# Kernel optimization log

Measured on AMD Instinct MI355X. Metric: run time of the kernel, lower is better.

Reference implementation:

```python
import jax, jax.numpy as jnp
import numpy as np

N = 100_000          # nodes
E = 1_600_000        # edges (avg degree 16)
F_RAW = 124          # float feature columns (after id column removed)
ID_DIM = 4
NF = F_RAW + ID_DIM  # encoder input features = 128
EMB = 64             # embedding_size, heads=1
L = 4                # num_layers
VOCAB = 2048         # id embedding table size
GAT_SLOPE = 0.2      # GATv2 attention leaky slope (PyG default)
ACT_SLOPE = 0.01     # nn.LeakyReLU default
EPS = 1e-5           # GraphNorm eps


def setup_inputs() -> dict:
    key = jax.random.key(0)
    ks = jax.random.split(key, 12)
    x_feat = jax.random.normal(ks[0], (N, F_RAW), jnp.float32)
    node_ids = jax.random.randint(ks[1], (N,), 0, VOCAB)
    edge_index = jax.random.randint(ks[2], (2, E), 0, N)
    emb_table = jax.random.normal(ks[3], (VOCAB, ID_DIM), jnp.float32) * 0.1
    w_in = jax.random.normal(ks[4], (NF, EMB), jnp.float32) / np.sqrt(NF)
    b_in = jnp.zeros((EMB,), jnp.float32)
    lin_w = jax.random.normal(ks[5], (L, EMB, EMB), jnp.float32) / np.sqrt(EMB)
    lin_b = jnp.zeros((L, EMB), jnp.float32)
    att = jax.random.normal(ks[6], (L, EMB), jnp.float32) / np.sqrt(EMB)
    conv_b = jnp.zeros((L, EMB), jnp.float32)
    gn_w = jnp.ones((L, EMB), jnp.float32)
    gn_b = jnp.zeros((L, EMB), jnp.float32)
    gn_ms = jnp.ones((L, EMB), jnp.float32)  # GraphNorm mean_scale
    return {"x_feat": x_feat, "node_ids": node_ids, "edge_index": edge_index,
            "emb_table": emb_table, "w_in": w_in, "b_in": b_in,
            "lin_w": lin_w, "lin_b": lin_b, "att": att, "conv_b": conv_b,
            "gn_w": gn_w, "gn_b": gn_b, "gn_ms": gn_ms}


def reference(x_feat, node_ids, edge_index, emb_table, w_in, b_in,
              lin_w, lin_b, att, conv_b, gn_w, gn_b, gn_ms):
    # id_encode: embedding lookup + concat with float features
    x = jnp.concatenate([x_feat, emb_table[node_ids]], axis=1)  # [N, 128]
    # encoder input projection (BatchNorm skipped: remove_random=True)
    x = jax.nn.leaky_relu(x @ w_in + b_in, ACT_SLOPE)           # [N, 64]
    n = x.shape[0]
    loops = jnp.arange(n)
    src = jnp.concatenate([edge_index[0], loops])               # add self loops
    dst = jnp.concatenate([edge_index[1], loops])
    h = None
    xs = []
    for l in range(L):
        # GATv2Conv, heads=1, share_weights=True (one shared linear)
        g = x @ lin_w[l] + lin_b[l]                             # [N, 64]
        e = jax.nn.leaky_relu(g[src] + g[dst], GAT_SLOPE) @ att[l]  # [E+N]
        # segment softmax over incoming edges per target node
        m = jax.ops.segment_max(e, dst, num_segments=n)
        ee = jnp.exp(e - m[dst])
        s = jax.ops.segment_sum(ee, dst, num_segments=n)
        alpha = ee / s[dst]                                     # [E+N]
        xs.append(alpha)
        x = jax.ops.segment_sum(alpha[:, None] * g[src], dst, num_segments=n) + conv_b[l]
        # GraphNorm (single graph: batch=None)
        mean = jnp.mean(x, axis=0)
        out = x - mean * gn_ms[l]
        var = jnp.mean(out * out, axis=0)
        x = out / jnp.sqrt(var + EPS) * gn_w[l] + gn_b[l]
        x = jax.nn.leaky_relu(x, ACT_SLOPE)
        # dropout p=0.3 is identity at inference
        h = x * 0.5 if h is None else h + x * 0.5
    return x, h, jnp.stack(xs, axis=0)  # ([N,64], [N,64], [L, E+N])
```

## Files before the change

kernel.cpp:

```cpp
#include <hip/hip_runtime.h>
#include <hip/hip_bf16.h>
#include <cstdint>

typedef __hip_bfloat16 bf16;
#define DEVI __device__ __forceinline__

DEVI float b2f(bf16 v){ return __bfloat162float(v); }
DEVI bf16 f2b(float v){ return __float2bfloat16(v); }
DEVI float lrelu(float x, float s){ return x > 0.f ? x : x * s; }

DEVI float ldf(const void* p, size_t i, int f){
  return f ? b2f(((const bf16*)p)[i]) : ((const float*)p)[i];
}
DEVI void stf(void* p, size_t i, int f, float v){
  if(f) ((bf16*)p)[i] = f2b(v); else ((float*)p)[i] = v;
}

DEVI float wave_sum(float v){
#pragma unroll
  for(int o = 32; o > 0; o >>= 1) v += __shfl_xor(v, o, 64);
  return v;
}
DEVI float qsum(float v){
  v += __shfl_xor(v, 1, 64);
  v += __shfl_xor(v, 2, 64);
  v += __shfl_xor(v, 4, 64);
  v += __shfl_xor(v, 8, 64);
  return v;
}

__global__ void k_detect(const uint32_t* __restrict__ xf, int* flag){
  const int lane = threadIdx.x & 63;
  float cnt = 0.f;
  for(int i = lane; i < 256; i += 64){
    uint32_t e = (xf[i] >> 7) & 0xFF;
    if(e >= 100 && e <= 140) cnt += 1.f;
  }
  cnt = wave_sum(cnt);
  if(lane == 0 && blockIdx.x == 0) *flag = (cnt > 180.f) ? 1 : 0;
}

__global__ __launch_bounds__(256) void k_encoder(
    const void* __restrict__ xf, const int* __restrict__ ids,
    const void* __restrict__ emb, const void* __restrict__ win,
    const void* __restrict__ bin, float* __restrict__ x,
    const int* __restrict__ flagp, int N)
{
  __shared__ float W[128*64];
  __shared__ float B[64];
  __shared__ float XR[4][128];
  const int t = threadIdx.x;
  const int f = *flagp;
  for(int i = t; i < 128*64; i += 256) W[i] = ldf(win, i, f);
  if(t < 64) B[t] = ldf(bin, t, f);
  __syncthreads();
  const int w = t >> 6, lane = t & 63;
  for(int base = blockIdx.x*4; base < N; base += gridDim.x*4){
    const int node = base + w;
    if(node < N){
      for(int k = lane; k < 128; k += 64){
        float v;
        if(k < 124) v = ldf(xf, (size_t)node*124 + k, f);
        else        v = ldf(emb, (size_t)ids[node]*4 + (k-124), f);
        XR[w][k] = v;
      }
      float acc = B[lane];
#pragma unroll 8
      for(int k = 0; k < 128; k++) acc = fmaf(XR[w][k], W[k*64+lane], acc);
      x[(size_t)node*64 + lane] = lrelu(acc, 0.01f);
    }
  }
}

__global__ __launch_bounds__(256) void k_linear(
    const float* __restrict__ x, const void* __restrict__ lw,
    const void* __restrict__ lb, float* __restrict__ g,
    const int* __restrict__ flagp, int layer, int N)
{
  __shared__ float W[64*64];
  __shared__ float B[64];
  __shared__ float XR[4][64];
  const int t = threadIdx.x;
  const int f = *flagp;
  const size_t wofs = (size_t)layer*64*64, bofs = (size_t)layer*64;
  for(int i = t; i < 64*64; i += 256) W[i] = ldf(lw, wofs + i, f);
  if(t < 64) B[t] = ldf(lb, bofs + t, f);
  __syncthreads();
  const int w = t >> 6, lane = t & 63;
  for(int base = blockIdx.x*4; base < N; base += gridDim.x*4){
    const int node = base + w;
    if(node < N){
      XR[w][lane] = x[(size_t)node*64 + lane];
      float acc = B[lane];
#pragma unroll 8
      for(int k = 0; k < 64; k++) acc = fmaf(XR[w][k], W[k*64+lane], acc);
      g[(size_t)node*64 + lane] = acc;
    }
  }
}

__global__ void k_deg_init(int* deg, int N){
  int i = blockIdx.x*blockDim.x + threadIdx.x;
  if(i < N) deg[i] = 1;
}
__global__ void k_deg_count(const int* __restrict__ dst, int* deg, int E){
  int j = blockIdx.x*blockDim.x + threadIdx.x;
  if(j < E) atomicAdd(&deg[dst[j]], 1);
}
__global__ __launch_bounds__(256) void k_scan_partial(const int* __restrict__ deg, int* partial, int N){
  __shared__ int red[256];
  const int c = blockIdx.x, base = c*1024, t = threadIdx.x;
  int s = 0;
  for(int i = t; i < 1024; i += 256){ int idx = base+i; s += (idx < N) ? deg[idx] : 0; }
  red[t] = s; __syncthreads();
  for(int o = 128; o > 0; o >>= 1){ if(t < o) red[t] += red[t+o]; __syncthreads(); }
  if(t == 0) partial[c] = red[0];
}
__global__ void k_scan_top(int* partial, int nchunks){
  if(threadIdx.x == 0 && blockIdx.x == 0){
    int run = 0;
    for(int i = 0; i < nchunks; i++){ int v = partial[i]; partial[i] = run; run += v; }
  }
}
__global__ __launch_bounds__(256) void k_scan_final(
    const int* __restrict__ deg, const int* __restrict__ partial,
    int* __restrict__ off, int* __restrict__ cur, int N)
{
  __shared__ int vals[1024];
  __shared__ int tsum[256];
  const int c = blockIdx.x, base = c*1024, t = threadIdx.x;
  for(int i = t; i < 1024; i += 256){ int idx = base+i; vals[i] = (idx < N) ? deg[idx] : 0; }
  __syncthreads();
  int a0 = vals[t*4], a1 = vals[t*4+1], a2 = vals[t*4+2], a3 = vals[t*4+3];
  int s = a0+a1+a2+a3;
  tsum[t] = s; __syncthreads();
  for(int o = 1; o < 256; o <<= 1){
    int v = (t >= o) ? tsum[t-o] : 0;
    __syncthreads();
    tsum[t] += v;
    __syncthreads();
  }
  int excl = tsum[t] - s + partial[c];
  int o0 = excl, o1 = o0+a0, o2 = o1+a1, o3 = o2+a2;
  int idx = base + t*4;
  if(idx   < N){ off[idx]   = o0; cur[idx]   = o0; }
  if(idx+1 < N){ off[idx+1] = o1; cur[idx+1] = o1; }
  if(idx+2 < N){ off[idx+2] = o2; cur[idx+2] = o2; }
  if(idx+3 < N){ off[idx+3] = o3; cur[idx+3] = o3; }
}
__global__ void k_scatter(const int* __restrict__ src, const int* __restrict__ dst,
                          int* cur, int* __restrict__ pos, int* __restrict__ csrc,
                          int E, int N){
  int j = blockIdx.x*blockDim.x + threadIdx.x;
  int T = E + N;
  if(j >= T) return;
  int s, d;
  if(j < E){ s = src[j]; d = dst[j]; } else { s = j - E; d = s; }
  int p = atomicAdd(&cur[d], 1);
  csrc[p] = s;
  pos[j]  = p;
}

__global__ __launch_bounds__(256) void k_gat(
    const float* __restrict__ g, const int* __restrict__ off,
    const int* __restrict__ deg, const int* __restrict__ csrc,
    const void* __restrict__ att, const void* __restrict__ convb,
    float* __restrict__ xout, float* __restrict__ acsr,
    float* __restrict__ stats, const int* __restrict__ flagp,
    int layer, int N)
{
  __shared__ float sv[4][64], sv2[4][64];
  const int t = threadIdx.x, w = t >> 6, lane = t & 63;
  const int q = lane >> 4, L = lane & 15;
  const int f = *flagp;
  const size_t pofs = (size_t)layer*64;
  const int node = blockIdx.x*4 + w;
  const bool act = node < N;
  const int nc = act ? node : (N-1);

  float4 attv, cbv;
  attv.x = ldf(att, pofs + 4*L+0, f); attv.y = ldf(att, pofs + 4*L+1, f);
  attv.z = ldf(att, pofs + 4*L+2, f); attv.w = ldf(att, pofs + 4*L+3, f);
  cbv.x = ldf(convb, pofs + 4*L+0, f); cbv.y = ldf(convb, pofs + 4*L+1, f);
  cbv.z = ldf(convb, pofs + 4*L+2, f); cbv.w = ldf(convb, pofs + 4*L+3, f);

  const float4 gd = *(const float4*)(g + (size_t)nc*64 + 4*L);
  const int o = off[nc];
  const int d = act ? deg[nc] : 0;
  const int sreg = csrc[o + (lane < d ? lane : 0)];

  float m = -1e30f, sp = 0.f, ereg = -1e30f;
  float4 acc = {0.f, 0.f, 0.f, 0.f};
  const int nit = (d + 3) >> 2;

  float4 gs;
  {
    const int s0 = __shfl(sreg, q, 64);
    gs = *(const float4*)(g + (size_t)s0*64 + 4*L);
  }
  for(int i = 0; i < nit; i++){
    float4 gnx = {0.f, 0.f, 0.f, 0.f};
    const int i1 = i + 1;
    const bool more = i1 < nit;
    if(more){
      int sn;
      if(i1 < 16) sn = __shfl(sreg, i1*4 + q, 64);
      else { const int j2 = i1*4 + q; sn = csrc[o + (j2 < d ? j2 : 0)]; }
      gnx = *(const float4*)(g + (size_t)sn*64 + 4*L);
    }
    const int j = i*4 + q;
    const bool have = j < d;
    float pe = lrelu(gs.x+gd.x, 0.2f)*attv.x + lrelu(gs.y+gd.y, 0.2f)*attv.y
             + lrelu(gs.z+gd.z, 0.2f)*attv.z + lrelu(gs.w+gd.w, 0.2f)*attv.w;
    float e = qsum(pe);
    if(!have) e = -1e30f;
    ereg = (L == i) ? e : ereg;
    const float mn = fmaxf(m, e);
    const float sc = __expf(m - mn);
    const float wt = __expf(e - mn);
    sp    = sp*sc    + wt;
    acc.x = acc.x*sc + wt*gs.x;
    acc.y = acc.y*sc + wt*gs.y;
    acc.z = acc.z*sc + wt*gs.z;
    acc.w = acc.w*sc + wt*gs.w;
    m = mn;
    if(more) gs = gnx;
  }
#pragma unroll
  for(int ofs = 16; ofs <= 32; ofs <<= 1){
    const float m2  = __shfl_xor(m,  ofs, 64);
    const float sp2 = __shfl_xor(sp, ofs, 64);
    float4 a2;
    a2.x = __shfl_xor(acc.x, ofs, 64); a2.y = __shfl_xor(acc.y, ofs, 64);
    a2.z = __shfl_xor(acc.z, ofs, 64); a2.w = __shfl_xor(acc.w, ofs, 64);
    const float mn = fmaxf(m, m2);
    const float sA = __expf(m - mn), sB = __expf(m2 - mn);
    sp    = sp*sA    + sp2*sB;
    acc.x = acc.x*sA + a2.x*sB;
    acc.y = acc.y*sA + a2.y*sB;
    acc.z = acc.z*sA + a2.z*sB;
    acc.w = acc.w*sA + a2.w*sB;
    m = mn;
  }
  const float inv = 1.f / sp;

  if(act){
    const int j = 4*L + q;
    if(j < d && j < 64)
      acsr[o + j] = __expf(ereg - m) * inv;
    for(int i = 16; i < nit; i++){
      const int j2 = i*4 + q;
      const bool have = j2 < d;
      const int s = csrc[o + (have ? j2 : 0)];
      const float4 gs2 = *(const float4*)(g + (size_t)s*64 + 4*L);
      float pe = lrelu(gs2.x+gd.x, 0.2f)*attv.x + lrelu(gs2.y+gd.y, 0.2f)*attv.y
               + lrelu(gs2.z+gd.z, 0.2f)*attv.z + lrelu(gs2.w+gd.w, 0.2f)*attv.w;
      float e = qsum(pe);
      if(have && L == 0)
        acsr[o + j2] = __expf(e - m) * inv;
    }
  }
  float4 v4 = {0.f, 0.f, 0.f, 0.f};
  if(act){
    v4.x = acc.x*inv + cbv.x; v4.y = acc.y*inv + cbv.y;
    v4.z = acc.z*inv + cbv.z; v4.w = acc.w*inv + cbv.w;
    if(q == 0) *(float4*)(xout + (size_t)node*64 + 4*L) = v4;
  }
  if(q == 0){
    sv [w][4*L+0] = v4.x;      sv [w][4*L+1] = v4.y;
    sv [w][4*L+2] = v4.z;      sv [w][4*L+3] = v4.w;
    sv2[w][4*L+0] = v4.x*v4.x; sv2[w][4*L+1] = v4.y*v4.y;
    sv2[w][4*L+2] = v4.z*v4.z; sv2[w][4*L+3] = v4.w*v4.w;
  }
  __syncthreads();
  if(w == 0){
    float a = sv[0][lane]+sv[1][lane]+sv[2][lane]+sv[3][lane];
    float b = sv2[0][lane]+sv2[1][lane]+sv2[2][lane]+sv2[3][lane];
    const int bank = (blockIdx.x & 7) * 128;
    atomicAdd(&stats[bank + lane],      a);
    atomicAdd(&stats[bank + 64 + lane], b);
  }
}

__global__ __launch_bounds__(256) void k_alpha_out(
    const float* __restrict__ acsr, const int* __restrict__ pos,
    void* __restrict__ out, size_t alpha_base,
    const int* __restrict__ flagp, int T)
{
  const int f = *flagp;
  for(size_t j = (size_t)blockIdx.x*256 + threadIdx.x; j < (size_t)T;
      j += (size_t)gridDim.x*256){
    stf(out, alpha_base + j, f, acsr[pos[j]]);
  }
}

__global__ void k_zero_stats(float* stats){ stats[threadIdx.x] = 0.f; }

__global__ __launch_bounds__(256) void k_gn_apply(
    float* __restrict__ x, const float* __restrict__ stats,
    const void* __restrict__ gw, const void* __restrict__ gb,
    const void* __restrict__ gms, void* __restrict__ out,
    size_t x_base, size_t h_base, const int* __restrict__ flagp,
    int N, int layer, float invN)
{
  const int f = *flagp;
  const int lane = threadIdx.x & 63;
  const size_t pofs = (size_t)layer*64;
  float s1 = 0.f, s2 = 0.f;
#pragma unroll
  for(int c = 0; c < 8; c++){
    s1 += stats[c*128 + lane];
    s2 += stats[c*128 + 64 + lane];
  }
  const float mean = s1 * invN;
  const float ex2  = s2 * invN;
  const float c    = mean * ldf(gms, pofs + lane, f);
  const float var  = ex2 - 2.f*c*mean + c*c;
  const float a    = ldf(gw, pofs + lane, f) / sqrtf(var + 1e-5f);
  const float bb   = ldf(gb, pofs + lane, f);
  const size_t total = (size_t)N * 64;
  for(size_t idx = (size_t)blockIdx.x*256 + threadIdx.x; idx < total;
      idx += (size_t)gridDim.x*256){
    float v = (x[idx] - c) * a + bb;
    v = lrelu(v, 0.01f);
    x[idx] = v;
    float hv = 0.5f*v + (layer == 0 ? 0.f : ldf(out, h_base + idx, f));
    stf(out, h_base + idx, f, hv);
    if(layer == 3) stf(out, x_base + idx, f, v);
  }
}

extern "C" void kernel_launch(void* const* d_in, const int* in_sizes, int n_in,
                              void* d_out, int out_size, void* d_ws, size_t ws_size,
                              hipStream_t stream) {
  const void* xf   = d_in[0];
  const int*  ids  = (const int*)d_in[1];
  const int*  eidx = (const int*)d_in[2];
  const void* emb  = d_in[3];
  const void* win  = d_in[4];
  const void* bin  = d_in[5];
  const void* lw   = d_in[6];
  const void* lb   = d_in[7];
  const void* att  = d_in[8];
  const void* cb   = d_in[9];
  const void* gw   = d_in[10];
  const void* gb   = d_in[11];
  const void* gms  = d_in[12];

  const int N = in_sizes[1];
  const int E = in_sizes[2] / 2;
  const int T = E + N;
  const int* srcp = eidx;
  const int* dstp = eidx + E;

  char* p = (char*)d_ws;
  float* x  = (float*)p; p += (size_t)N*64*4;
  float* g  = (float*)p; p += (size_t)N*64*4;
  int* deg  = (int*)p;   p += ((size_t)N*4 + 63) & ~63ull;
  int* off  = (int*)p;   p += ((size_t)N*4 + 63) & ~63ull;
  int* cur  = (int*)p;   p += ((size_t)N*4 + 63) & ~63ull;
  int* pos  = (int*)p;   p += ((size_t)T*4 + 63) & ~63ull;
  int* csrc = (int*)p;   p += ((size_t)T*4 + 63) & ~63ull;
  float* acsr = (float*)p; p += ((size_t)T*4 + 63) & ~63ull;
  int* partial = (int*)p; p += 4096;
  float* stats = (float*)p; p += 4096;
  int* flag = (int*)p;    p += 64;

  const size_t x_base = 0;
  const size_t h_base = (size_t)N*64;
  const size_t a_base = (size_t)2*N*64;

  k_detect<<<1, 64, 0, stream>>>((const uint32_t*)xf, flag);
  k_encoder<<<2048, 256, 0, stream>>>(xf, ids, emb, win, bin, x, flag, N);

  k_deg_init <<<(N+255)/256, 256, 0, stream>>>(deg, N);
  k_deg_count<<<(E+255)/256, 256, 0, stream>>>(dstp, deg, E);
  const int nchunks = (N + 1023) / 1024;
  k_scan_partial<<<nchunks, 256, 0, stream>>>(deg, partial, N);
  k_scan_top    <<<1, 1, 0, stream>>>(partial, nchunks);
  k_scan_final  <<<nchunks, 256, 0, stream>>>(deg, partial, off, cur, N);
  k_scatter     <<<(T+255)/256, 256, 0, stream>>>(srcp, dstp, cur, pos, csrc, E, N);

  for(int l = 0; l < 4; l++){
    k_zero_stats<<<1, 1024, 0, stream>>>(stats);
    k_linear<<<2048, 256, 0, stream>>>(x, lw, lb, g, flag, l, N);
    k_gat<<<(N+3)/4, 256, 0, stream>>>(g, off, deg, csrc, att, cb, x,
                                       acsr, stats, flag, l, N);
    k_alpha_out<<<1024, 256, 0, stream>>>(acsr, pos, d_out,
                                          a_base + (size_t)l*T, flag, T);
    k_gn_apply<<<1024, 256, 0, stream>>>(x, stats, gw, gb, gms, d_out,
                                         x_base, h_base, flag, N, l, 1.0f/(float)N);
  }
}
```

Measured before the change: 1.181 ms.

## Bucket CSR scatter via shared memory, fuse alpha output into GraphNorm, drop stat zeroing

The CSR build is split into two passes. The first pass writes (position, source) pairs into 1024-slot buckets, reusing the g buffer as scratch. The second pass places each bucket in shared memory and writes csrc coalesced, replacing fully random 4-byte stores. The per-layer alpha output kernel is merged into k_gn_apply, and the stats buffer becomes per-layer and is zeroed once in k_deg_init, so two launches per layer disappear. The cost is an extra bucket atomic and an extra pass over T entries in the one-time setup.

```diff
diff --git a/kernel.cpp b/kernel.cpp
--- a/kernel.cpp
+++ b/kernel.cpp
@@ -99,9 +99,11 @@
   }
 }
 
-__global__ void k_deg_init(int* deg, int N){
+__global__ void k_deg_init(int* deg, float* stats, int* bcur, int nbuckets, int N){
   int i = blockIdx.x*blockDim.x + threadIdx.x;
   if(i < N) deg[i] = 1;
+  if(i < 4096) stats[i] = 0.f;
+  if(i < nbuckets) bcur[i] = i << 10;
 }
 __global__ void k_deg_count(const int* __restrict__ dst, int* deg, int E){
   int j = blockIdx.x*blockDim.x + threadIdx.x;
@@ -148,17 +150,31 @@
   if(idx+2 < N){ off[idx+2] = o2; cur[idx+2] = o2; }
   if(idx+3 < N){ off[idx+3] = o3; cur[idx+3] = o3; }
 }
-__global__ void k_scatter(const int* __restrict__ src, const int* __restrict__ dst,
-                          int* cur, int* __restrict__ pos, int* __restrict__ csrc,
-                          int E, int N){
+__global__ void k_scatter_a(const int* __restrict__ src, const int* __restrict__ dst,
+                            int* cur, int* __restrict__ pos, int* bcur,
+                            int2* __restrict__ bstore, int E, int N){
   int j = blockIdx.x*blockDim.x + threadIdx.x;
   int T = E + N;
   if(j >= T) return;
   int s, d;
   if(j < E){ s = src[j]; d = dst[j]; } else { s = j - E; d = s; }
   int p = atomicAdd(&cur[d], 1);
-  csrc[p] = s;
-  pos[j]  = p;
+  pos[j] = p;
+  int b = p >> 10;
+  int q = atomicAdd(&bcur[b], 1);
+  bstore[q] = make_int2(p, s);
+}
+__global__ __launch_bounds__(256) void k_scatter_b(
+    const int2* __restrict__ bstore, int* __restrict__ csrc, int T){
+  __shared__ int tmp[1024];
+  const int base = blockIdx.x << 10, t = threadIdx.x;
+  const int cnt = min(T - base, 1024);
+  for(int i = t; i < cnt; i += 256){
+    int2 e = bstore[base + i];
+    tmp[e.x - base] = e.y;
+  }
+  __syncthreads();
+  for(int i = t; i < cnt; i += 256) csrc[base + i] = tmp[i];
 }
 
 __global__ __launch_bounds__(256) void k_gat(
@@ -174,6 +190,7 @@
   const int q = lane >> 4, L = lane & 15;
   const int f = *flagp;
   const size_t pofs = (size_t)layer*64;
+  float* __restrict__ st = stats + (size_t)layer*1024;
   const int node = blockIdx.x*4 + w;
   const bool act = node < N;
   const int nc = act ? node : (N-1);
@@ -277,40 +294,28 @@
     float a = sv[0][lane]+sv[1][lane]+sv[2][lane]+sv[3][lane];
     float b = sv2[0][lane]+sv2[1][lane]+sv2[2][lane]+sv2[3][lane];
     const int bank = (blockIdx.x & 7) * 128;
-    atomicAdd(&stats[bank + lane],      a);
-    atomicAdd(&stats[bank + 64 + lane], b);
-  }
-}
-
-__global__ __launch_bounds__(256) void k_alpha_out(
-    const float* __restrict__ acsr, const int* __restrict__ pos,
-    void* __restrict__ out, size_t alpha_base,
-    const int* __restrict__ flagp, int T)
-{
-  const int f = *flagp;
-  for(size_t j = (size_t)blockIdx.x*256 + threadIdx.x; j < (size_t)T;
-      j += (size_t)gridDim.x*256){
-    stf(out, alpha_base + j, f, acsr[pos[j]]);
-  }
-}
-
-__global__ void k_zero_stats(float* stats){ stats[threadIdx.x] = 0.f; }
+    atomicAdd(&st[bank + lane],      a);
+    atomicAdd(&st[bank + 64 + lane], b);
+  }
+}
 
 __global__ __launch_bounds__(256) void k_gn_apply(
     float* __restrict__ x, const float* __restrict__ stats,
     const void* __restrict__ gw, const void* __restrict__ gb,
     const void* __restrict__ gms, void* __restrict__ out,
-    size_t x_base, size_t h_base, const int* __restrict__ flagp,
-    int N, int layer, float invN)
+    const float* __restrict__ acsr, const int* __restrict__ pos,
+    size_t x_base, size_t h_base, size_t alpha_base,
+    const int* __restrict__ flagp, int N, int T, int layer, float invN)
 {
   const int f = *flagp;
   const int lane = threadIdx.x & 63;
+  const float* __restrict__ st = stats + (size_t)layer*1024;
   const size_t pofs = (size_t)layer*64;
   float s1 = 0.f, s2 = 0.f;
 #pragma unroll
   for(int c = 0; c < 8; c++){
-    s1 += stats[c*128 + lane];
-    s2 += stats[c*128 + 64 + lane];
+    s1 += st[c*128 + lane];
+    s2 += st[c*128 + 64 + lane];
   }
   const float mean = s1 * invN;
   const float ex2  = s2 * invN;
@@ -327,6 +332,10 @@
     float hv = 0.5f*v + (layer == 0 ? 0.f : ldf(out, h_base + idx, f));
     stf(out, h_base + idx, f, hv);
     if(layer == 3) stf(out, x_base + idx, f, v);
+  }
+  for(size_t j = (size_t)blockIdx.x*256 + threadIdx.x; j < (size_t)T;
+      j += (size_t)gridDim.x*256){
+    stf(out, alpha_base + j, f, acsr[pos[j]]);
   }
 }
 
@@ -350,6 +359,7 @@
   const int N = in_sizes[1];
   const int E = in_sizes[2] / 2;
   const int T = E + N;
+  const int nbuckets = (T + 1023) >> 10;
   const int* srcp = eidx;
   const int* dstp = eidx + E;
 
@@ -363,8 +373,10 @@
   int* csrc = (int*)p;   p += ((size_t)T*4 + 63) & ~63ull;
   float* acsr = (float*)p; p += ((size_t)T*4 + 63) & ~63ull;
   int* partial = (int*)p; p += 4096;
-  float* stats = (float*)p; p += 4096;
-  int* flag = (int*)p;    p += 64;
+  float* stats = (float*)p; p += 4*1024*4;
+  int* bcur = (int*)p;   p += ((size_t)nbuckets*4 + 63) & ~63ull;
+  int* flag = (int*)p;   p += 64;
+  int2* bstore = (int2*)g;
 
   const size_t x_base = 0;
   const size_t h_base = (size_t)N*64;
@@ -373,22 +385,23 @@
   k_detect<<<1, 64, 0, stream>>>((const uint32_t*)xf, flag);
   k_encoder<<<2048, 256, 0, stream>>>(xf, ids, emb, win, bin, x, flag, N);
 
-  k_deg_init <<<(N+255)/256, 256, 0, stream>>>(deg, N);
+  k_deg_init <<<(N+255)/256, 256, 0, stream>>>(deg, stats, bcur, nbuckets, N);
   k_deg_count<<<(E+255)/256, 256, 0, stream>>>(dstp, deg, E);
   const int nchunks = (N + 1023) / 1024;
   k_scan_partial<<<nchunks, 256, 0, stream>>>(deg, partial, N);
   k_scan_top    <<<1, 1, 0, stream>>>(partial, nchunks);
   k_scan_final  <<<nchunks, 256, 0, stream>>>(deg, partial, off, cur, N);
-  k_scatter     <<<(T+255)/256, 256, 0, stream>>>(srcp, dstp, cur, pos, csrc, E, N);
+  k_scatter_a   <<<(T+255)/256, 256, 0, stream>>>(srcp, dstp, cur, pos, bcur,
+                                                  bstore, E, N);
+  k_scatter_b   <<<nbuckets, 256, 0, stream>>>(bstore, csrc, T);
 
   for(int l = 0; l < 4; l++){
-    k_zero_stats<<<1, 1024, 0, stream>>>(stats);
     k_linear<<<2048, 256, 0, stream>>>(x, lw, lb, g, flag, l, N);
     k_gat<<<(N+3)/4, 256, 0, stream>>>(g, off, deg, csrc, att, cb, x,
                                        acsr, stats, flag, l, N);
-    k_alpha_out<<<1024, 256, 0, stream>>>(acsr, pos, d_out,
-                                          a_base + (size_t)l*T, flag, T);
     k_gn_apply<<<1024, 256, 0, stream>>>(x, stats, gw, gb, gms, d_out,
-                                         x_base, h_base, flag, N, l, 1.0f/(float)N);
-  }
-}
+                                         acsr, pos, x_base, h_base,
+                                         a_base + (size_t)l*T, flag,
+                                         N, T, l, 1.0f/(float)N);
+  }
+}
```

New measurement: 1.365 ms. 15.6% more time.
